# Optimization experiments

Hardware: AMD Instinct MI355X
Metric: run time of the kernel (lower is better)

## Reference

```python
import jax, jax.numpy as jnp
import numpy as np

KERNEL = 3
STRIDE = 1


def _extract_patches(x, k, stride):
    """x: (b, h, w, *rest) -> (b, oh, ow, k, k, *rest). VALID padding."""
    b, h, w = x.shape[0], x.shape[1], x.shape[2]
    oh = (h - k) // stride + 1
    ow = (w - k) // stride + 1
    rows = []
    for ky in range(k):
        cols = []
        for kx in range(k):
            cols.append(x[:, ky:ky + stride * (oh - 1) + 1:stride,
                           kx:kx + stride * (ow - 1) + 1:stride])
        rows.append(jnp.stack(cols, axis=3))  # (b, oh, ow, kx, *rest)
    return jnp.stack(rows, axis=3)            # (b, oh, ow, ky, kx, *rest)


def setup_inputs() -> dict:
    key = jax.random.key(0)
    k1, k2, k3 = jax.random.split(key, 3)
    poses = jax.random.normal(k1, (4, 16, 16, 32, 4, 4), dtype=jnp.float32)
    activations = jax.random.uniform(k2, (4, 16, 16, 32, 1, 1), dtype=jnp.float32)
    # learned param: (k, k, in_caps, out_caps, sqrt_atom, sqrt_atom)
    pose_kernel = jax.random.normal(k3, (3, 3, 32, 32, 4, 4), dtype=jnp.float32)
    return {"poses": poses, "activations": activations, "pose_kernel": pose_kernel}


def reference(poses, activations, pose_kernel):
    k = pose_kernel.shape[0]
    # Poses -> votes: patch extraction then per-capsule 4x4 matmul broadcast.
    pose_patches = _extract_patches(poses, k, STRIDE)       # (b,oh,ow,k,k,i,m,n)
    votes = jnp.einsum('bhwxyimn,xyiomn->bhwxyiomn', pose_patches, pose_kernel)
    # Activations: patches with an inserted out-capsule broadcast axis at -3.
    act_patches = _extract_patches(activations, k, STRIDE)  # (b,oh,ow,k,k,i,1,1)
    act_out = jnp.expand_dims(act_patches, -3)              # (b,oh,ow,k,k,i,1,1,1)
    return votes, act_out
```

## Files before the change

kernel.cpp:

```cpp
#include <hip/hip_runtime.h>


#define V4_COUNT 28901376
#define A4_COUNT 56448

__global__ __launch_bounds__(256) void convcaps_kernel(
    const float4* __restrict__ poses,
    const float4* __restrict__ acts,
    const float4* __restrict__ pk,
    float4* __restrict__ out) {

    unsigned idx = blockIdx.x * 256u + threadIdx.x;

    if (idx < V4_COUNT) {
        unsigned e4 = idx & 3u;
        unsigned o  = (idx >> 2) & 31u;
        unsigned i  = (idx >> 7) & 31u;
        unsigned r  = idx >> 12;
        unsigned kx = r % 3u;  r /= 3u;
        unsigned ky = r % 3u;  r /= 3u;
        unsigned w  = r % 14u; r /= 14u;
        unsigned h  = r % 14u; r /= 14u;
        unsigned b  = r;

        float4 p = poses[(((b * 16u + h + ky) * 16u + (w + kx)) * 32u + i) * 4u + e4];
        float4 k = pk[(((ky * 3u + kx) * 32u + i) * 32u + o) * 4u + e4];

        float4 v;
        v.x = p.x * k.x;
        v.y = p.y * k.y;
        v.z = p.z * k.z;
        v.w = p.w * k.w;
        out[idx] = v;
    } else if (idx < V4_COUNT + A4_COUNT) {
        unsigned a  = idx - V4_COUNT;
        unsigned i4 = a & 7u;
        unsigned r  = a >> 3;
        unsigned kx = r % 3u;  r /= 3u;
        unsigned ky = r % 3u;  r /= 3u;
        unsigned w  = r % 14u; r /= 14u;
        unsigned h  = r % 14u; r /= 14u;
        unsigned b  = r;
        out[idx] = acts[((b * 16u + h + ky) * 16u + (w + kx)) * 8u + i4];
    }
}

extern "C" void kernel_launch(void* const* d_in, const int* in_sizes, int n_in,
                              void* d_out, int out_size, void* d_ws, size_t ws_size,
                              hipStream_t stream) {
    const float4* poses = (const float4*)d_in[0];
    const float4* acts  = (const float4*)d_in[1];
    const float4* pk    = (const float4*)d_in[2];
    float4* out         = (float4*)d_out;

    const unsigned total = V4_COUNT + A4_COUNT;
    const unsigned blocks = (total + 255u) / 256u;
    convcaps_kernel<<<blocks, 256, 0, stream>>>(poses, acts, pk, out);
}
```

Baseline: 475.5 us.

## Assign one block per patch slot and use nontemporal stores

Each block now handles a whole (b,h,w,ky,kx) slot of 4096 float4 outputs, looping 16 times over input capsules. The index decomposition is done once per block instead of once per thread, and the activation patch copy is folded into the same blocks. Output writes use nontemporal stores so the write-only output stream does not pollute the caches. This cuts integer divide work and launch size, but lowers the number of blocks and adds a serial loop per thread.

```diff
diff --git a/kernel.cpp b/kernel.cpp
--- a/kernel.cpp
+++ b/kernel.cpp
@@ -1,59 +1,59 @@
 #include <hip/hip_runtime.h>
 
 
-#define V4_COUNT 28901376
-#define A4_COUNT 56448
+typedef float v4f __attribute__((ext_vector_type(4)));
+
+#define SLOTS    7056u
+#define V4_COUNT 28901376u
+#define A4_COUNT 56448u
 
 __global__ __launch_bounds__(256) void convcaps_kernel(
-    const float4* __restrict__ poses,
-    const float4* __restrict__ acts,
-    const float4* __restrict__ pk,
-    float4* __restrict__ out) {
+    const v4f* __restrict__ poses,
+    const v4f* __restrict__ acts,
+    const v4f* __restrict__ pk,
+    v4f* __restrict__ out) {
 
-    unsigned idx = blockIdx.x * 256u + threadIdx.x;
+    const unsigned blk = blockIdx.x;
+    const unsigned t   = threadIdx.x;
 
-    if (idx < V4_COUNT) {
-        unsigned e4 = idx & 3u;
-        unsigned o  = (idx >> 2) & 31u;
-        unsigned i  = (idx >> 7) & 31u;
-        unsigned r  = idx >> 12;
-        unsigned kx = r % 3u;  r /= 3u;
-        unsigned ky = r % 3u;  r /= 3u;
-        unsigned w  = r % 14u; r /= 14u;
-        unsigned h  = r % 14u; r /= 14u;
-        unsigned b  = r;
+    unsigned r  = blk;
+    unsigned kx = r % 3u;  r /= 3u;
+    unsigned ky = r % 3u;  r /= 3u;
+    unsigned w  = r % 14u; r /= 14u;
+    unsigned h  = r % 14u; r /= 14u;
+    unsigned b  = r;
 
-        float4 p = poses[(((b * 16u + h + ky) * 16u + (w + kx)) * 32u + i) * 4u + e4];
-        float4 k = pk[(((ky * 3u + kx) * 32u + i) * 32u + o) * 4u + e4];
+    const unsigned src_pix = (b * 16u + h + ky) * 16u + (w + kx);
+    const v4f* __restrict__ pbase = poses + (size_t)src_pix * 128u;
+    const v4f* __restrict__ kbase = pk    + (size_t)(ky * 3u + kx) * 4096u;
+    v4f* __restrict__ obase       = out   + (size_t)blk * 4096u;
 
-        float4 v;
-        v.x = p.x * k.x;
-        v.y = p.y * k.y;
-        v.z = p.z * k.z;
-        v.w = p.w * k.w;
-        out[idx] = v;
-    } else if (idx < V4_COUNT + A4_COUNT) {
-        unsigned a  = idx - V4_COUNT;
-        unsigned i4 = a & 7u;
-        unsigned r  = a >> 3;
-        unsigned kx = r % 3u;  r /= 3u;
-        unsigned ky = r % 3u;  r /= 3u;
-        unsigned w  = r % 14u; r /= 14u;
-        unsigned h  = r % 14u; r /= 14u;
-        unsigned b  = r;
-        out[idx] = acts[((b * 16u + h + ky) * 16u + (w + kx)) * 8u + i4];
+    const unsigned e4 = t & 3u;
+    const unsigned o  = (t >> 2) & 31u;
+    const unsigned i0 = t >> 7;
+
+    #pragma unroll
+    for (unsigned it = 0; it < 16u; ++it) {
+        const unsigned i = i0 + 2u * it;
+        v4f p = pbase[i * 4u + e4];
+        v4f k = kbase[(i * 32u + o) * 4u + e4];
+        v4f v = p * k;
+        __builtin_nontemporal_store(v, &obase[it * 256u + t]);
+    }
+
+    if (t < 8u) {
+        v4f a = acts[(size_t)src_pix * 8u + t];
+        __builtin_nontemporal_store(a, &out[V4_COUNT + blk * 8u + t]);
     }
 }
 
 extern "C" void kernel_launch(void* const* d_in, const int* in_sizes, int n_in,
                               void* d_out, int out_size, void* d_ws, size_t ws_size,
                               hipStream_t stream) {
-    const float4* poses = (const float4*)d_in[0];
-    const float4* acts  = (const float4*)d_in[1];
-    const float4* pk    = (const float4*)d_in[2];
-    float4* out         = (float4*)d_out;
+    const v4f* poses = (const v4f*)d_in[0];
+    const v4f* acts  = (const v4f*)d_in[1];
+    const v4f* pk    = (const v4f*)d_in[2];
+    v4f* out         = (v4f*)d_out;
 
-    const unsigned total = V4_COUNT + A4_COUNT;
-    const unsigned blocks = (total + 255u) / 256u;
-    convcaps_kernel<<<blocks, 256, 0, stream>>>(poses, acts, pk, out);
+    convcaps_kernel<<<SLOTS, 256, 0, stream>>>(poses, acts, pk, out);
 }
```

Measured after the change: 472.8 us. No clear change (-0.6%).
